# Kernel optimization log

Hardware: AMD Instinct MI355X
Metric: run time of the kernel (lower is better)

## Reference

```python
import jax, jax.numpy as jnp
import numpy as np

HEADS, DIM_HEAD, LANDMARKS, PINV_ITERS, RES_K = 8, 64, 256, 6, 33
DIM = 512


def layer_norm(x, w, b, eps=1e-5):
    mu = x.mean(-1, keepdims=True)
    var = ((x - mu) ** 2).mean(-1, keepdims=True)
    return (x - mu) * jax.lax.rsqrt(var + eps) * w + b


def moore_penrose_pinv(x, iters=PINV_ITERS):
    # x: (b, h, m, m)
    abs_x = jnp.abs(x)
    col = abs_x.sum(-1)
    row = abs_x.sum(-2)
    z = jnp.swapaxes(x, -1, -2) / (jnp.max(col) * jnp.max(row))
    I = jnp.eye(x.shape[-1], dtype=x.dtype)
    for _ in range(iters):
        xz = x @ z
        z = 0.25 * z @ (13.0 * I - xz @ (15.0 * I - xz @ (7.0 * I - xz)))
    return z


def nystrom_attention(x, qkv_w, out_w, out_b, res_kernel):
    b, n, _ = x.shape
    h, dh, m = HEADS, DIM_HEAD, LANDMARKS
    l = n // m  # seq chosen divisible by landmarks
    qkv = x @ qkv_w  # (b, n, 3*h*dh)
    q, k, v = jnp.split(qkv, 3, axis=-1)
    def to_heads(t):
        return t.reshape(b, n, h, dh).transpose(0, 2, 1, 3)  # (b,h,n,dh)
    q, k, v = to_heads(q), to_heads(k), to_heads(v)
    q = q * (dh ** -0.5)
    # landmark pooling: mean over contiguous groups of size l
    q_l = q.reshape(b, h, m, l, dh).mean(axis=3)  # (b,h,m,dh)
    k_l = k.reshape(b, h, m, l, dh).mean(axis=3)
    attn1 = jax.nn.softmax(jnp.einsum('bhid,bhjd->bhij', q, k_l), axis=-1)   # (b,h,n,m)
    attn2 = jax.nn.softmax(jnp.einsum('bhid,bhjd->bhij', q_l, k_l), axis=-1) # (b,h,m,m)
    attn3 = jax.nn.softmax(jnp.einsum('bhid,bhjd->bhij', q_l, k), axis=-1)   # (b,h,m,n)
    attn2_inv = moore_penrose_pinv(attn2)
    out = (attn1 @ attn2_inv) @ (attn3 @ v)  # (b,h,n,dh)
    # depthwise residual conv over sequence dim, per head
    pad = (RES_K - 1) // 2
    out = out + jax.lax.conv_general_dilated(
        v, res_kernel, window_strides=(1, 1), padding=((pad, pad), (0, 0)),
        dimension_numbers=('NCHW', 'OIHW', 'NCHW'), feature_group_count=h)
    out = out.transpose(0, 2, 1, 3).reshape(b, n, h * dh)
    return out @ out_w + out_b


def trans_layer(x, p):
    return x + nystrom_attention(layer_norm(x, p['norm_w'], p['norm_b']),
                                 p['qkv_w'], p['out_w'], p['out_b'], p['res_k'])


def setup_inputs() -> dict:
    key = jax.random.key(0)
    ks = jax.random.split(key, 20)
    N, F = 16383, 1024
    d = {}
    d['x'] = jax.random.normal(ks[0], (1, N, F), dtype=jnp.float32)
    d['fc_w'] = jax.random.normal(ks[1], (F, DIM), dtype=jnp.float32) * 0.03
    d['fc_b'] = jnp.zeros((DIM,), dtype=jnp.float32)
    d['cls_token'] = jax.random.normal(ks[2], (1, 1, DIM), dtype=jnp.float32) * 1e-6
    for i, base in [(3, 'l1'), (9, 'l2')]:
        d[base + '_norm_w'] = jnp.ones((DIM,), dtype=jnp.float32)
        d[base + '_norm_b'] = jnp.zeros((DIM,), dtype=jnp.float32)
        d[base + '_qkv_w'] = jax.random.normal(ks[i], (DIM, 3 * DIM), dtype=jnp.float32) * 0.03
        d[base + '_out_w'] = jax.random.normal(ks[i + 1], (DIM, DIM), dtype=jnp.float32) * 0.03
        d[base + '_out_b'] = jnp.zeros((DIM,), dtype=jnp.float32)
        d[base + '_res_k'] = jax.random.normal(ks[i + 2], (HEADS, 1, RES_K, 1), dtype=jnp.float32) * 0.1
    d['norm_w'] = jnp.ones((DIM,), dtype=jnp.float32)
    d['norm_b'] = jnp.zeros((DIM,), dtype=jnp.float32)
    d['clf_w'] = jax.random.normal(ks[15], (DIM, 4), dtype=jnp.float32) * 0.05
    d['clf_b'] = jnp.zeros((4,), dtype=jnp.float32)
    return d


def reference(x, fc_w, fc_b, cls_token, l1_norm_w, l1_norm_b, l1_qkv_w, l1_out_w,
              l1_out_b, l1_res_k, l2_norm_w, l2_norm_b, l2_qkv_w, l2_out_w,
              l2_out_b, l2_res_k, norm_w, norm_b, clf_w, clf_b):
    h = jax.nn.relu(x @ fc_w + fc_b)                       # (1, N, 512)
    h = jnp.concatenate([cls_token, h], axis=1)            # (1, N+1, 512)
    p1 = dict(norm_w=l1_norm_w, norm_b=l1_norm_b, qkv_w=l1_qkv_w,
              out_w=l1_out_w, out_b=l1_out_b, res_k=l1_res_k)
    p2 = dict(norm_w=l2_norm_w, norm_b=l2_norm_b, qkv_w=l2_qkv_w,
              out_w=l2_out_w, out_b=l2_out_b, res_k=l2_res_k)
    h = trans_layer(h, p1)
    h = trans_layer(h, p2)
    h = layer_norm(h, norm_w, norm_b)[:, 0]                # (1, 512)
    logits = h @ clf_w + clf_b                             # (1, n_classes)
    hazards = jax.nn.sigmoid(logits)
    S = jnp.cumprod(1.0 - hazards, axis=1)
    return (hazards, S)
```

## Files before the change

kernel.cpp:

```cpp
#include <hip/hip_runtime.h>

#define NTOK 16384
#define NDIM 512
#define STP_LD 280

typedef __attribute__((ext_vector_type(8))) short short8;
typedef __attribute__((ext_vector_type(4))) float f32x4;

__device__ __forceinline__ unsigned short f2bf(float f) {
  unsigned u = __float_as_uint(f);
  u += 0x7fffu + ((u >> 16) & 1u);
  return (unsigned short)(u >> 16);
}
__device__ __forceinline__ float bf2f(unsigned short u) {
  return __uint_as_float((unsigned)u << 16);
}

__device__ __forceinline__ void gload_lds16(const void* g, void* l) {
  __builtin_amdgcn_global_load_lds(
      (const __attribute__((address_space(1))) unsigned int*)(unsigned long long)(g),
      (__attribute__((address_space(3))) unsigned int*)(unsigned long long)(l), 16, 0, 0);
}

template<int EPI>
__global__ __launch_bounds__(256) void gemm_bf16(
    const unsigned short* __restrict__ A, const unsigned short* __restrict__ Bt,
    float* __restrict__ C, const float* __restrict__ bias,
    int M, int N, int K, int Mstore)
{
  __shared__ unsigned short As[2][128 * 32];
  __shared__ unsigned short Bs[2][128 * 32];
  const int tid = threadIdx.x;
  const int id = blockIdx.y * gridDim.x + blockIdx.x;
  const int nwg8 = (gridDim.x * gridDim.y) >> 3;
  const int logical = (id & 7) * nwg8 + (id >> 3);
  const int row0 = (logical / gridDim.x) * 128;
  const int col0 = (logical % gridDim.x) * 128;
  const int wave = tid >> 6, lane = tid & 63;
  const int wm = (wave >> 1) * 64, wn = (wave & 1) * 64;
  const int quad = lane >> 4, m16 = lane & 15;

  const int r0 = tid >> 2;
  const int c8 = (tid & 3) * 8;
  const unsigned short* Ag0 = A + (size_t)(row0 + r0) * K + c8;
  const unsigned short* Ag1 = A + (size_t)(row0 + r0 + 64) * K + c8;
  const unsigned short* Bg0 = Bt + (size_t)(col0 + r0) * K + c8;
  const unsigned short* Bg1 = Bt + (size_t)(col0 + r0 + 64) * K + c8;
  char* AsB = (char*)As;
  char* BsB = (char*)Bs;
  const int wb = wave * 1024;

  f32x4 acc[4][4] = {};
  const int nc = K >> 5;
  gload_lds16(Ag0, AsB + wb);
  gload_lds16(Ag1, AsB + 4096 + wb);
  gload_lds16(Bg0, BsB + wb);
  gload_lds16(Bg1, BsB + 4096 + wb);
  __syncthreads();
  int b = 0;
  for (int c = 0; c < nc; c++) {
    if (c + 1 < nc) {
      int k1 = (c + 1) * 32;
      gload_lds16(Ag0 + k1, AsB + (b ^ 1) * 8192 + wb);
      gload_lds16(Ag1 + k1, AsB + (b ^ 1) * 8192 + 4096 + wb);
      gload_lds16(Bg0 + k1, BsB + (b ^ 1) * 8192 + wb);
      gload_lds16(Bg1 + k1, BsB + (b ^ 1) * 8192 + 4096 + wb);
    }
    short8 af[4], bf[4];
#pragma unroll
    for (int i = 0; i < 4; i++) {
      af[i] = *(const short8*)&As[b][(wm + i * 16 + m16) * 32 + quad * 8];
      bf[i] = *(const short8*)&Bs[b][(wn + i * 16 + m16) * 32 + quad * 8];
    }
#pragma unroll
    for (int i = 0; i < 4; i++)
#pragma unroll
      for (int j = 0; j < 4; j++)
        acc[i][j] = __builtin_amdgcn_mfma_f32_16x16x32_bf16(af[i], bf[j], acc[i][j], 0, 0, 0);
    __syncthreads();
    b ^= 1;
  }
#pragma unroll
  for (int i = 0; i < 4; i++) {
#pragma unroll
    for (int r = 0; r < 4; r++) {
      int gr = row0 + wm + i * 16 + quad * 4 + r;
      if (gr < Mstore) {
#pragma unroll
        for (int j = 0; j < 4; j++) {
          int gc = col0 + wn + j * 16 + m16;
          float v = acc[i][j][r];
          if (EPI == 1) { v += bias[gc]; v = fmaxf(v, 0.f); }
          if (EPI == 2) { v += bias[gc] + C[(size_t)gr * N + gc]; }
          C[(size_t)gr * N + gc] = v;
        }
      }
    }
  }
}

__global__ __launch_bounds__(256) void qkv_gemm(
    const unsigned short* __restrict__ A, const unsigned short* __restrict__ Bt,
    unsigned short* __restrict__ qb, unsigned short* __restrict__ kb,
    unsigned short* __restrict__ vTb,
    float* __restrict__ q_l, float* __restrict__ k_lT,
    unsigned short* __restrict__ q_lb, unsigned short* __restrict__ k_lb)
{
  __shared__ unsigned short smem[17408];
  unsigned short* AsU = smem;
  unsigned short* BsU = smem + 8192;
  unsigned short* vt  = smem;
  const int tid = threadIdx.x;
  const int id = blockIdx.y * gridDim.x + blockIdx.x;
  const int nwg8 = (gridDim.x * gridDim.y) >> 3;
  const int logical = (id & 7) * nwg8 + (id >> 3);
  const int bx = logical % 12, by = logical / 12;
  const int row0 = by * 128, col0 = bx * 128;
  const int wave = tid >> 6, lane = tid & 63;
  const int wm = (wave >> 1) * 64, wn = (wave & 1) * 64;
  const int quad = lane >> 4, m16 = lane & 15;

  const int r0 = tid >> 2;
  const int c8 = (tid & 3) * 8;
  const unsigned short* Ag0 = A + (size_t)(row0 + r0) * 512 + c8;
  const unsigned short* Ag1 = A + (size_t)(row0 + r0 + 64) * 512 + c8;
  const unsigned short* Bg0 = Bt + (size_t)(col0 + r0) * 512 + c8;
  const unsigned short* Bg1 = Bt + (size_t)(col0 + r0 + 64) * 512 + c8;
  char* AsB = (char*)AsU;
  char* BsB = (char*)BsU;
  const int wb = wave * 1024;

  f32x4 acc[4][4] = {};
  gload_lds16(Ag0, AsB + wb);
  gload_lds16(Ag1, AsB + 4096 + wb);
  gload_lds16(Bg0, BsB + wb);
  gload_lds16(Bg1, BsB + 4096 + wb);
  __syncthreads();
  int b = 0;
  for (int c = 0; c < 16; c++) {
    if (c < 15) {
      int k1 = (c + 1) * 32;
      gload_lds16(Ag0 + k1, AsB + (b ^ 1) * 8192 + wb);
      gload_lds16(Ag1 + k1, AsB + (b ^ 1) * 8192 + 4096 + wb);
      gload_lds16(Bg0 + k1, BsB + (b ^ 1) * 8192 + wb);
      gload_lds16(Bg1 + k1, BsB + (b ^ 1) * 8192 + 4096 + wb);
    }
    short8 af[4], bf[4];
#pragma unroll
    for (int i = 0; i < 4; i++) {
      af[i] = *(const short8*)&AsU[b * 4096 + (wm + i * 16 + m16) * 32 + quad * 8];
      bf[i] = *(const short8*)&BsU[b * 4096 + (wn + i * 16 + m16) * 32 + quad * 8];
    }
#pragma unroll
    for (int i = 0; i < 4; i++)
#pragma unroll
      for (int j = 0; j < 4; j++)
        acc[i][j] = __builtin_amdgcn_mfma_f32_16x16x32_bf16(af[i], bf[j], acc[i][j], 0, 0, 0);
    __syncthreads();
    b ^= 1;
  }

  const int sel = bx >> 2;
  if (sel == 2) {
#pragma unroll
    for (int i = 0; i < 4; i++)
#pragma unroll
      for (int j = 0; j < 4; j++) {
        int c_l = wn + j * 16 + m16;
        int r_b = wm + i * 16 + quad * 4;
        ushort4 o;
        o.x = f2bf(acc[i][j][0]); o.y = f2bf(acc[i][j][1]);
        o.z = f2bf(acc[i][j][2]); o.w = f2bf(acc[i][j][3]);
        *(ushort4*)&vt[c_l * 136 + r_b] = o;
      }
    __syncthreads();
    const int gc0 = col0 - 1024;
    const int u = tid & 15, cc = tid >> 4;
#pragma unroll
    for (int pass = 0; pass < 8; pass++) {
      int c = pass * 16 + cc;
      short8 v8 = *(const short8*)&vt[c * 136 + u * 8];
      *(short8*)(vTb + (size_t)(gc0 + c) * NTOK + row0 + u * 8) = v8;
    }
  } else {
    const bool isq = (sel == 0);
    const float mul = isq ? 0.125f : 1.f;
#pragma unroll
    for (int i = 0; i < 4; i++)
#pragma unroll
      for (int j = 0; j < 4; j++) {
        int lc = wn + j * 16 + m16;
#pragma unroll
        for (int r = 0; r < 4; r++) {
          int lr = wm + i * 16 + quad * 4 + r;
          vt[lr * 136 + lc] = f2bf(acc[i][j][r] * mul);
        }
      }
    float ps[4];
#pragma unroll
    for (int j = 0; j < 4; j++) {
      float s = 0.f;
#pragma unroll
      for (int i = 0; i < 4; i++)
#pragma unroll
        for (int r = 0; r < 4; r++) s += acc[i][j][r];
      s += __shfl_xor(s, 16);
      s += __shfl_xor(s, 32);
      ps[j] = s;
    }
    if (quad == 0) {
      const int jg = by * 2 + (wm >> 6);
      const float sc = isq ? (0.125f / 64.f) : (1.f / 64.f);
#pragma unroll
      for (int j = 0; j < 4; j++) {
        int gc = col0 + wn + j * 16 + m16 - (isq ? 0 : 512);
        int hh = gc >> 6, d = gc & 63;
        float p = ps[j] * sc;
        if (isq) {
          size_t o = ((size_t)(hh * 256 + jg)) * 64 + d;
          q_l[o] = p;
          q_lb[o] = f2bf(p);
        } else {
          k_lT[((size_t)hh * 64 + d) * 256 + jg] = p;
          size_t of = ((size_t)hh << 14) + (jg >> 6) * 4096 + (d >> 5) * 2048
                    + ((jg >> 4) & 3) * 512 + ((d >> 3) & 3) * 128 + (jg & 15) * 8 + (d & 7);
          k_lb[of] = f2bf(p);
        }
      }
    }
    __syncthreads();
    unsigned short* ob = isq ? (qb + (size_t)row0 * 512 + col0)
                             : (kb + (size_t)row0 * 512 + (col0 - 512));
    const int u = tid & 15, cc = tid >> 4;
#pragma unroll
    for (int pass = 0; pass < 8; pass++) {
      int rloc = pass * 16 + cc;
      short8 v8 = *(const short8*)&vt[rloc * 136 + u * 8];
      *(short8*)(ob + (size_t)rloc * 512 + u * 8) = v8;
    }
  }
}

template<bool WN, bool WT, bool WF>
__global__ __launch_bounds__(256) void bmm_pinv64(
    const unsigned short* __restrict__ A, const unsigned short* __restrict__ Bt,
    unsigned short* __restrict__ Cn, unsigned short* __restrict__ Ct,
    float* __restrict__ Cf,
    float an, float bn, float at, float bt)
{
  const int hh = blockIdx.z;
  A  += (size_t)hh << 16;
  Bt += (size_t)hh << 16;
  __shared__ unsigned short As[2][64 * 32];
  __shared__ unsigned short Bs[2][64 * 32];
  const int tid = threadIdx.x;
  const int row0 = blockIdx.y * 64, col0 = blockIdx.x * 64;
  const int wave = tid >> 6, lane = tid & 63;
  const int wm = (wave >> 1) * 32, wn = (wave & 1) * 32;
  const int quad = lane >> 4, m16 = lane & 15;
  const int sr = wave * 16 + (lane >> 2);
  const int sc = (lane & 3) * 8;
  const unsigned short* Ag = A + (size_t)(row0 + sr) * 256 + sc;
  const unsigned short* Bg = Bt + (size_t)(col0 + sr) * 256 + sc;
  char* AsW = (char*)As + wave * 1024;
  char* BsW = (char*)Bs + wave * 1024;

  f32x4 acc[2][2] = {};
  gload_lds16(Ag, AsW);
  gload_lds16(Bg, BsW);
  __syncthreads();
  int b = 0;
  for (int c = 0; c < 8; c++) {
    if (c < 7) {
      gload_lds16(Ag + (c + 1) * 32, AsW + (b ^ 1) * 4096);
      gload_lds16(Bg + (c + 1) * 32, BsW + (b ^ 1) * 4096);
    }
    short8 af[2], bfr[2];
#pragma unroll
    for (int i = 0; i < 2; i++) {
      af[i]  = *(const short8*)&As[b][(wm + i * 16 + m16) * 32 + quad * 8];
      bfr[i] = *(const short8*)&Bs[b][(wn + i * 16 + m16) * 32 + quad * 8];
    }
#pragma unroll
    for (int i = 0; i < 2; i++)
#pragma unroll
      for (int j = 0; j < 2; j++)
        acc[i][j] = __builtin_amdgcn_mfma_f32_16x16x32_bf16(af[i], bfr[j], acc[i][j], 0, 0, 0);
    __syncthreads();
    b ^= 1;
  }
  unsigned short* CnH = Cn + ((size_t)hh << 16);
  unsigned short* CtH = Ct + ((size_t)hh << 16);
  float* CfH = WF ? (Cf + ((size_t)hh << 16)) : nullptr;
#pragma unroll
  for (int i = 0; i < 2; i++) {
#pragma unroll
    for (int r = 0; r < 4; r++) {
      int gr = row0 + wm + i * 16 + quad * 4 + r;
#pragma unroll
      for (int j = 0; j < 2; j++) {
        int gc = col0 + wn + j * 16 + m16;
        float p = acc[i][j][r];
        float diag = (gr == gc) ? 1.f : 0.f;
        if (WN) {
          unsigned short nb_ = f2bf(an * p + bn * diag);
          CnH[(size_t)gr * 256 + gc] = nb_;
          if (WF) CfH[(size_t)gr * 256 + gc] = bf2f(nb_);
        }
        if (WT) CtH[(size_t)gc * 256 + gr] = f2bf(at * p + bt * diag);
      }
    }
  }
}

__global__ void castpad_x(const float* __restrict__ x, unsigned short* __restrict__ xb,
                          size_t nvalid, const float* __restrict__ cls,
                          float* __restrict__ h) {
  size_t i4 = ((size_t)blockIdx.x * 256 + threadIdx.x) * 4;
  float4 v = make_float4(0.f, 0.f, 0.f, 0.f);
  if (i4 < nvalid) v = *(const float4*)(x + i4);
  ushort4 o;
  o.x = f2bf(v.x); o.y = f2bf(v.y); o.z = f2bf(v.z); o.w = f2bf(v.w);
  *(ushort4*)(xb + i4) = o;
  if (blockIdx.x == 0 && threadIdx.x < 128)
    *(float4*)(h + threadIdx.x * 4) = *(const float4*)(cls + threadIdx.x * 4);
}

__global__ __launch_bounds__(256) void transpose_cast(
    const float* __restrict__ in, unsigned short* __restrict__ out, int R, int C)
{
  __shared__ float tile[32][33];
  int r0 = blockIdx.x * 32, c0 = blockIdx.y * 32;
  int tx = threadIdx.x & 31, ty = threadIdx.x >> 5;
  for (int yy = ty; yy < 32; yy += 8)
    tile[yy][tx] = in[(size_t)(r0 + yy) * C + c0 + tx];
  __syncthreads();
  for (int yy = ty; yy < 32; yy += 8)
    out[(size_t)(c0 + yy) * R + r0 + tx] = f2bf(tile[tx][yy]);
}

__global__ __launch_bounds__(256) void conv_seq(
    const unsigned short* __restrict__ vTb, const float* __restrict__ res_k,
    unsigned short* __restrict__ convT)
{
  const int c = blockIdx.y;
  const int h = c >> 6;
  const int i0 = (blockIdx.x * 256 + threadIdx.x) * 8;
  float rk[33];
#pragma unroll
  for (int u = 0; u < 33; u++) rk[u] = res_k[h * 33 + u];
  const unsigned short* vr = vTb + (size_t)c * NTOK;
  float win[40];
#pragma unroll
  for (int ch = 0; ch < 5; ch++) {
    int a = i0 - 16 + ch * 8;
    if (a >= 0 && a < NTOK) {
      ushort4 u0 = *(const ushort4*)(vr + a);
      ushort4 u1 = *(const ushort4*)(vr + a + 4);
      win[ch * 8 + 0] = bf2f(u0.x); win[ch * 8 + 1] = bf2f(u0.y);
      win[ch * 8 + 2] = bf2f(u0.z); win[ch * 8 + 3] = bf2f(u0.w);
      win[ch * 8 + 4] = bf2f(u1.x); win[ch * 8 + 5] = bf2f(u1.y);
      win[ch * 8 + 6] = bf2f(u1.z); win[ch * 8 + 7] = bf2f(u1.w);
    } else {
#pragma unroll
      for (int u = 0; u < 8; u++) win[ch * 8 + u] = 0.f;
    }
  }
  ushort4 o0, o1;
  float out[8];
#pragma unroll
  for (int jj = 0; jj < 8; jj++) {
    float s = 0.f;
#pragma unroll
    for (int u = 0; u < 33; u++) s += rk[u] * win[jj + u];
    out[jj] = s;
  }
  o0.x = f2bf(out[0]); o0.y = f2bf(out[1]); o0.z = f2bf(out[2]); o0.w = f2bf(out[3]);
  o1.x = f2bf(out[4]); o1.y = f2bf(out[5]); o1.z = f2bf(out[6]); o1.w = f2bf(out[7]);
  *(ushort4*)(convT + (size_t)c * NTOK + i0) = o0;
  *(ushort4*)(convT + (size_t)c * NTOK + i0 + 4) = o1;
}

template<bool W2>
__global__ __launch_bounds__(256) void bmm_f32(
    const float* __restrict__ A, const float* __restrict__ B, float* __restrict__ C,
    float* __restrict__ C2, int M, int N, int K, float alpha, float beta, float gamma)
{
  const int h = blockIdx.z;
  A += (size_t)h * M * K; B += (size_t)h * K * N;
  size_t cb = (size_t)h * M * N;
  __shared__ float As[16][64];
  __shared__ float Bs[16][64];
  const int tid = threadIdx.x;
  const int row0 = blockIdx.y * 64, col0 = blockIdx.x * 64;
  const int ty = tid >> 4, tx = tid & 15;
  const int ar = tid >> 2, ac = (tid & 3) << 2;
  const int bk = tid >> 4, bj = (tid & 15) << 2;
  float acc[4][4] = {};
  float4 a  = *(const float4*)(A + (size_t)(row0 + ar) * K + ac);
  float4 bv = *(const float4*)(B + (size_t)bk * N + col0 + bj);
  for (int k0 = 0; k0 < K; k0 += 16) {
    As[ac + 0][ar] = a.x; As[ac + 1][ar] = a.y; As[ac + 2][ar] = a.z; As[ac + 3][ar] = a.w;
    *(float4*)&Bs[bk][bj] = bv;
    __syncthreads();
    if (k0 + 16 < K) {
      a  = *(const float4*)(A + (size_t)(row0 + ar) * K + k0 + 16 + ac);
      bv = *(const float4*)(B + (size_t)(k0 + 16 + bk) * N + col0 + bj);
    }
#pragma unroll
    for (int kk = 0; kk < 16; kk++) {
      float4 av = *(float4*)&As[kk][ty << 2];
      float4 bvv = *(float4*)&Bs[kk][tx << 2];
      float a4[4] = {av.x, av.y, av.z, av.w};
      float b4[4] = {bvv.x, bvv.y, bvv.z, bvv.w};
#pragma unroll
      for (int ii = 0; ii < 4; ii++)
#pragma unroll
        for (int jj = 0; jj < 4; jj++) acc[ii][jj] += a4[ii] * b4[jj];
    }
    __syncthreads();
  }
#pragma unroll
  for (int ii = 0; ii < 4; ii++) {
    int gr = row0 + (ty << 2) + ii;
#pragma unroll
    for (int jj = 0; jj < 4; jj++) {
      int gc = col0 + (tx << 2) + jj;
      float diag = (gr == gc) ? 1.f : 0.f;
      float v = alpha * acc[ii][jj] + beta * diag;
      C[cb + (size_t)gr * N + gc] = v;
      if (W2) C2[cb + (size_t)gr * N + gc] = gamma * diag - v;
    }
  }
}

__global__ __launch_bounds__(256) void layernorm_rows(
    const float* __restrict__ x, unsigned short* __restrict__ y,
    const float* __restrict__ w, const float* __restrict__ b)
{
  const int row = blockIdx.x, tid = threadIdx.x;
  const float* xr = x + (size_t)row * NDIM;
  float2 v = ((const float2*)xr)[tid];
  float sum = v.x + v.y, sq = v.x * v.x + v.y * v.y;
#pragma unroll
  for (int off = 32; off; off >>= 1) { sum += __shfl_xor(sum, off); sq += __shfl_xor(sq, off); }
  __shared__ float r1[4], r2[4];
  if ((tid & 63) == 0) { r1[tid >> 6] = sum; r2[tid >> 6] = sq; }
  __syncthreads();
  sum = r1[0] + r1[1] + r1[2] + r1[3];
  sq  = r2[0] + r2[1] + r2[2] + r2[3];
  float mu = sum * (1.f / 512.f);
  float var = sq * (1.f / 512.f) - mu * mu;
  float rs = rsqrtf(var + 1e-5f);
  float a = (v.x - mu) * rs * w[2 * tid]     + b[2 * tid];
  float c = (v.y - mu) * rs * w[2 * tid + 1] + b[2 * tid + 1];
  ((unsigned*)(y + (size_t)row * NDIM))[tid] = (unsigned)f2bf(a) | ((unsigned)f2bf(c) << 16);
}

__global__ __launch_bounds__(256) void attn2_softmax(
    const float* __restrict__ q_l, const float* __restrict__ k_lT,
    float* __restrict__ x2, unsigned short* __restrict__ x2b)
{
  int row = blockIdx.x, h = blockIdx.y, j = threadIdx.x;
// ... 124 lines not shown

  FF_STAGE(0, 0);
  __syncthreads();
  int b = 0;
  for (int c = 0; c < 8; c++) {
    if (c < 7) FF_STAGE(b ^ 1, c + 1);
    const unsigned short* Kb = Ks[b];
    const unsigned short* Vb = Vs[b];
    f32x4 s[4] = {};
    __builtin_amdgcn_s_setprio(1);
#pragma unroll
    for (int kt = 0; kt < 4; kt++) {
      const unsigned short* krow = Kb + ((kt << 4) + m16) * 64;
      short8 b0 = *(const short8*)(krow + co0);
      short8 b1 = *(const short8*)(krow + co1);
      s[kt] = __builtin_amdgcn_mfma_f32_16x16x32_bf16(aq0, b0, s[kt], 0, 0, 0);
      s[kt] = __builtin_amdgcn_mfma_f32_16x16x32_bf16(aq1, b1, s[kt], 0, 0, 0);
    }
    __builtin_amdgcn_s_setprio(0);
#pragma unroll
    for (int e = 0; e < 4; e++) {
      float mx = fmaxf(fmaxf(s[0][e], s[1][e]), fmaxf(s[2][e], s[3][e]));
      mx = fmaxf(mx, __shfl_xor(mx, 1));
      mx = fmaxf(mx, __shfl_xor(mx, 2));
      mx = fmaxf(mx, __shfl_xor(mx, 4));
      mx = fmaxf(mx, __shfl_xor(mx, 8));
      float mn = fmaxf(m_e[e], mx);
      float scale = __expf(m_e[e] - mn);
      m_e[e] = mn;
      float sum = 0.f;
#pragma unroll
      for (int kt = 0; kt < 4; kt++) {
        float ev = __expf(s[kt][e] - mn);
        s[kt][e] = ev;
        sum += ev;
      }
      sum += __shfl_xor(sum, 1); sum += __shfl_xor(sum, 2);
      sum += __shfl_xor(sum, 4); sum += __shfl_xor(sum, 8);
      l_e[e] = l_e[e] * scale + sum;
#pragma unroll
      for (int dt = 0; dt < 4; dt++) acc_o[dt][e] *= scale;
    }
#pragma unroll
    for (int kt = 0; kt < 4; kt++)
#pragma unroll
      for (int e = 0; e < 4; e++)
        pbuf[(quad * 4 + e) * 72 + kt * 16 + m16] = f2bf(s[kt][e]);
    asm volatile("s_waitcnt lgkmcnt(0)" ::: "memory");
    short8 ap0 = *(const short8*)&pbuf[m16 * 72 + quad * 8];
    short8 ap1 = *(const short8*)&pbuf[m16 * 72 + 32 + quad * 8];
    __builtin_amdgcn_s_setprio(1);
#pragma unroll
    for (int dt = 0; dt < 4; dt++) {
      const unsigned short* vrow = Vb + ((dt << 4) + m16) * 64;
      short8 bv0 = *(const short8*)(vrow + co0);
      short8 bv1 = *(const short8*)(vrow + co1);
      acc_o[dt] = __builtin_amdgcn_mfma_f32_16x16x32_bf16(ap0, bv0, acc_o[dt], 0, 0, 0);
      acc_o[dt] = __builtin_amdgcn_mfma_f32_16x16x32_bf16(ap1, bv1, acc_o[dt], 0, 0, 0);
    }
    __builtin_amdgcn_s_setprio(0);
    __syncthreads();
    b ^= 1;
  }
#undef FF_STAGE
  float* ob = Opart + ((size_t)(ks * 8 + h) * 256 + qrow_w) * 64;
#pragma unroll
  for (int dt = 0; dt < 4; dt++)
#pragma unroll
    for (int e = 0; e < 4; e++)
      ob[(size_t)(quad * 4 + e) * 64 + dt * 16 + m16] = acc_o[dt][e];
  if (m16 == 0) {
    float* mlb = mlpart + ((size_t)(ks * 8 + h) * 256 + qrow_w) * 2;
#pragma unroll
    for (int e = 0; e < 4; e++) {
      mlb[(quad * 4 + e) * 2]     = m_e[e];
      mlb[(quad * 4 + e) * 2 + 1] = l_e[e];
    }
  }
}

__global__ __launch_bounds__(256) void flash_merge(
    const float* __restrict__ Opart, const float* __restrict__ mlpart,
    float* __restrict__ kv)
{
  const int rc = blockIdx.x, h = blockIdx.y, tid = threadIdx.x;
  const int r = rc * 32 + (tid >> 3);
  const int d0 = (tid & 7) * 8;
  float M = -1e30f;
  for (int ks = 0; ks < 32; ks++)
    M = fmaxf(M, mlpart[((size_t)(ks * 8 + h) * 256 + r) * 2]);
  float L = 0.f;
  float o[8];
#pragma unroll
  for (int j = 0; j < 8; j++) o[j] = 0.f;
  for (int ks = 0; ks < 32; ks++) {
    const float* mlb = mlpart + ((size_t)(ks * 8 + h) * 256 + r) * 2;
    float w = __expf(mlb[0] - M);
    L += mlb[1] * w;
    const float* op = Opart + ((size_t)(ks * 8 + h) * 256 + r) * 64 + d0;
    float4 a = *(const float4*)op;
    float4 b = *(const float4*)(op + 4);
    o[0] += a.x * w; o[1] += a.y * w; o[2] += a.z * w; o[3] += a.w * w;
    o[4] += b.x * w; o[5] += b.y * w; o[6] += b.z * w; o[7] += b.w * w;
  }
  float invL = 1.f / L;
  float* out = kv + ((size_t)(h * 256 + r)) * 64 + d0;
#pragma unroll
  for (int j = 0; j < 8; j++) out[j] = o[j] * invL;
}

__global__ __launch_bounds__(256) void bmt_kernel(
    const float* __restrict__ zf, const float* __restrict__ kv,
    unsigned short* __restrict__ BmT)
{
  const int jb = blockIdx.x, hh = blockIdx.y, tid = threadIdx.x;
  __shared__ float zt[64 * 256];
  const float* zsrc = zf + ((size_t)hh << 16) + (size_t)(jb * 64) * 256;
  for (int rep = 0; rep < 16; rep++) {
    int e4 = (rep * 256 + tid) * 4;
    *(float4*)&zt[e4] = *(const float4*)(zsrc + e4);
  }
  __syncthreads();
  const int d = tid & 63, jg = tid >> 6;
  const float* kvh = kv + ((size_t)hh << 14) + d;
  float acc[16];
#pragma unroll
  for (int u = 0; u < 16; u++) acc[u] = 0.f;
  for (int k0 = 0; k0 < 256; k0 += 8) {
    float kv8[8];
#pragma unroll
    for (int u = 0; u < 8; u++) kv8[u] = kvh[(size_t)(k0 + u) << 6];
#pragma unroll
    for (int jj = 0; jj < 16; jj++) {
      const float* zr = &zt[(jg * 16 + jj) * 256 + k0];
#pragma unroll
      for (int u = 0; u < 8; u++) acc[jj] += zr[u] * kv8[u];
    }
  }
  unsigned short* obh = BmT + ((size_t)hh << 14) + (d >> 5) * 8192
                        + ((d >> 4) & 1) * 512 + (d & 15) * 8;
#pragma unroll
  for (int jj = 0; jj < 16; jj++) {
    int j = jb * 64 + jg * 16 + jj;
    obh[(j >> 5) * 1024 + ((j >> 3) & 3) * 128 + (j & 7)] = f2bf(acc[jj]);
  }
}

__global__ __launch_bounds__(256) void attn1_out(
    const unsigned short* __restrict__ qb, const unsigned short* __restrict__ k_lb,
    const unsigned short* __restrict__ BmT, const unsigned short* __restrict__ convT,
    unsigned short* __restrict__ attn_out)
{
  const int qc = blockIdx.x, h = blockIdx.y, tid = threadIdx.x;
  const int q0 = qc * 32;
  const int wave = tid >> 6, lane = tid & 63;
  const int quad = lane >> 4, m16 = lane & 15;

  __shared__ unsigned short stp[32 * STP_LD];
  __shared__ float redm[4][32], redl[4][32];

  const int mi3 = (wave & 1) * 16;
  const int nbase = (wave >> 1) * 32;
  const int gi0 = q0 + mi3 + quad * 4;
  ushort4 cv4_[2];
#pragma unroll
  for (int t = 0; t < 2; t++) {
    int d = nbase + t * 16 + m16;
    cv4_[t] = *(const ushort4*)(convT + (size_t)((h << 6) + d) * NTOK + gi0);
  }

  f32x4 acc1[2][4] = {};
  {
    const unsigned short* qbase = qb + (size_t)q0 * 512 + (h << 6);
    const unsigned short* kf = k_lb + ((size_t)h << 14) + (wave << 12);
#pragma unroll
    for (int kc = 0; kc < 2; kc++) {
      short8 aq[2], bk[4];
#pragma unroll
      for (int i = 0; i < 2; i++)
        aq[i] = *(const short8*)(qbase + (size_t)(i * 16 + m16) * 512 + kc * 32 + quad * 8);
#pragma unroll
      for (int n = 0; n < 4; n++)
        bk[n] = *(const short8*)(kf + kc * 2048 + n * 512 + lane * 8);
#pragma unroll
      for (int i = 0; i < 2; i++)
#pragma unroll
        for (int n = 0; n < 4; n++)
          acc1[i][n] = __builtin_amdgcn_mfma_f32_16x16x32_bf16(aq[i], bk[n], acc1[i][n], 0, 0, 0);
    }
  }
#pragma unroll
  for (int i = 0; i < 2; i++) {
#pragma unroll
    for (int e = 0; e < 4; e++) {
      float mx = fmaxf(fmaxf(acc1[i][0][e], acc1[i][1][e]), fmaxf(acc1[i][2][e], acc1[i][3][e]));
      mx = fmaxf(mx, __shfl_xor(mx, 1));
      mx = fmaxf(mx, __shfl_xor(mx, 2));
      mx = fmaxf(mx, __shfl_xor(mx, 4));
      mx = fmaxf(mx, __shfl_xor(mx, 8));
      if (m16 == 0) redm[wave][i * 16 + quad * 4 + e] = mx;
    }
  }
  __syncthreads();
#pragma unroll
  for (int i = 0; i < 2; i++) {
#pragma unroll
    for (int e = 0; e < 4; e++) {
      int r = i * 16 + quad * 4 + e;
      float gm = fmaxf(fmaxf(redm[0][r], redm[1][r]), fmaxf(redm[2][r], redm[3][r]));
      float s = 0.f;
#pragma unroll
      for (int n = 0; n < 4; n++) {
        float ev = __expf(acc1[i][n][e] - gm);
        acc1[i][n][e] = ev;
        s += ev;
      }
      s += __shfl_xor(s, 1); s += __shfl_xor(s, 2);
      s += __shfl_xor(s, 4); s += __shfl_xor(s, 8);
      if (m16 == 0) redl[wave][r] = s;
    }
  }
#pragma unroll
  for (int i = 0; i < 2; i++)
#pragma unroll
    for (int n = 0; n < 4; n++) {
      int col = wave * 64 + n * 16 + m16;
#pragma unroll
      for (int e = 0; e < 4; e++)
        stp[(i * 16 + quad * 4 + e) * STP_LD + col] = f2bf(acc1[i][n][e]);
    }
  __syncthreads();

  f32x4 acc3[2] = {};
  {
    const unsigned short* bf_ = BmT + ((size_t)h << 14) + ((nbase >> 5) << 13);
#pragma unroll
    for (int kc = 0; kc < 8; kc++) {
      short8 ap = *(const short8*)&stp[(mi3 + m16) * STP_LD + kc * 32 + quad * 8];
#pragma unroll
      for (int t = 0; t < 2; t++) {
        short8 bp = *(const short8*)(bf_ + kc * 1024 + t * 512 + lane * 8);
        acc3[t] = __builtin_amdgcn_mfma_f32_16x16x32_bf16(ap, bp, acc3[t], 0, 0, 0);
      }
    }
  }
#pragma unroll
  for (int t = 0; t < 2; t++) {
    int d = nbase + t * 16 + m16;
    unsigned short cvs[4] = {cv4_[t].x, cv4_[t].y, cv4_[t].z, cv4_[t].w};
#pragma unroll
    for (int e = 0; e < 4; e++) {
      int lr = mi3 + quad * 4 + e;
      float l = redl[0][lr] + redl[1][lr] + redl[2][lr] + redl[3][lr];
      float v = acc3[t][e] / l + bf2f(cvs[e]);
      attn_out[((size_t)(gi0 + e) << 9) + (h << 6) + d] = f2bf(v);
    }
  }
}

__global__ __launch_bounds__(256) void final_head(
    const float* __restrict__ hrow, const float* __restrict__ nw, const float* __restrict__ nb,
    const float* __restrict__ cw, const float* __restrict__ cb, float* __restrict__ out)
{
  const int tid = threadIdx.x;
  __shared__ float ln0[512];
  __shared__ float r1[4], r2[4];
  __shared__ float lg[4][4];
  float2 v = ((const float2*)hrow)[tid];
  float sum = v.x + v.y, sq = v.x * v.x + v.y * v.y;
#pragma unroll
  for (int off = 32; off; off >>= 1) { sum += __shfl_xor(sum, off); sq += __shfl_xor(sq, off); }
  if ((tid & 63) == 0) { r1[tid >> 6] = sum; r2[tid >> 6] = sq; }
  __syncthreads();
  sum = r1[0] + r1[1] + r1[2] + r1[3];
  sq  = r2[0] + r2[1] + r2[2] + r2[3];
  float mu = sum * (1.f / 512.f);
  float var = sq * (1.f / 512.f) - mu * mu;
  float rs = rsqrtf(var + 1e-5f);
  ln0[2 * tid]     = (v.x - mu) * rs * nw[2 * tid]     + nb[2 * tid];
  ln0[2 * tid + 1] = (v.y - mu) * rs * nw[2 * tid + 1] + nb[2 * tid + 1];
  __syncthreads();
  float p[4] = {0.f, 0.f, 0.f, 0.f};
  for (int k = tid; k < 512; k += 256) {
    float lv = ln0[k];
#pragma unroll
    for (int c = 0; c < 4; c++) p[c] += lv * cw[k * 4 + c];
  }
#pragma unroll
  for (int off = 32; off; off >>= 1)
#pragma unroll
    for (int c = 0; c < 4; c++) p[c] += __shfl_xor(p[c], off);
  if ((tid & 63) == 0) {
    int w = tid >> 6;
#pragma unroll
    for (int c = 0; c < 4; c++) lg[w][c] = p[c];
  }
  __syncthreads();
  if (tid == 0) {
    float cum = 1.f;
    for (int c = 0; c < 4; c++) {
      float logit = lg[0][c] + lg[1][c] + lg[2][c] + lg[3][c] + cb[c];
      float hz = 1.f / (1.f + __expf(-logit));
      out[c] = hz;
      cum *= (1.f - hz);
      out[4 + c] = cum;
    }
  }
}

extern "C" void kernel_launch(void* const* d_in, const int* in_sizes, int n_in,
                              void* d_out, int out_size, void* d_ws, size_t ws_size,
                              hipStream_t stream)
{
  (void)in_sizes; (void)n_in; (void)out_size; (void)ws_size;
  const float* x    = (const float*)d_in[0];
  const float* fc_w = (const float*)d_in[1];
  const float* fc_b = (const float*)d_in[2];
  const float* cls  = (const float*)d_in[3];
  const float* nw[2]   = {(const float*)d_in[4],  (const float*)d_in[10]};
  const float* nb[2]   = {(const float*)d_in[5],  (const float*)d_in[11]};
  const float* qkvw[2] = {(const float*)d_in[6],  (const float*)d_in[12]};
  const float* outw[2] = {(const float*)d_in[7],  (const float*)d_in[13]};
  const float* outb[2] = {(const float*)d_in[8],  (const float*)d_in[14]};
  const float* resk[2] = {(const float*)d_in[9],  (const float*)d_in[15]};
  const float* fnw = (const float*)d_in[16];
  const float* fnb = (const float*)d_in[17];
  const float* cw  = (const float*)d_in[18];
  const float* cb  = (const float*)d_in[19];

  float* ws = (float*)d_ws;
  float* h    = ws; ws += (size_t)NTOK * NDIM;
  float* qkv  = ws; ws += (size_t)NTOK * 1536;
  float* bigv = ws; ws += (size_t)(512 * NTOK) / 2;
  float* q_l  = ws; ws += 8 * 256 * 64;
  float* k_lT = ws; ws += 8 * 256 * 64;
  float* x2   = ws; ws += 8 * 256 * 256;
  float* zf   = ws; ws += 8 * 256 * 256;
  float* zfin = ws; ws += 8 * 256 * 256;
  float* tA   = ws; ws += 8 * 256 * 256;
  float* tB   = ws; ws += 8 * 256 * 256;
  float* tC   = ws; ws += 8 * 256 * 256;
  float* kv   = ws; ws += 8 * 256 * 64;
  float* scal = ws; ws += 64;
  unsigned short* actb = (unsigned short*)ws; ws += (size_t)NTOK * NDIM / 2;
  unsigned short* wT   = (unsigned short*)ws; ws += (1536 * 512) / 2;
  unsigned short* qb   = (unsigned short*)ws; ws += (size_t)NTOK * NDIM / 2;
  unsigned short* k_lb = (unsigned short*)ws; ws += (8 * 256 * 64) / 2;
  unsigned short* q_lb = (unsigned short*)ws; ws += (8 * 256 * 64) / 2;
  unsigned short* x2b  = (unsigned short*)ws; ws += (8 * 256 * 256) / 2;
  unsigned short* zb0  = (unsigned short*)ws; ws += (8 * 256 * 256) / 2;
  unsigned short* zb1  = (unsigned short*)ws; ws += (8 * 256 * 256) / 2;
  unsigned short* zT0  = (unsigned short*)ws; ws += (8 * 256 * 256) / 2;
  unsigned short* zT1  = (unsigned short*)ws; ws += (8 * 256 * 256) / 2;
  unsigned short* xzb  = (unsigned short*)ws; ws += (8 * 256 * 256) / 2;
  unsigned short* t1T  = (unsigned short*)ws; ws += (8 * 256 * 256) / 2;
  unsigned short* t2T  = (unsigned short*)ws; ws += (8 * 256 * 256) / 2;
  unsigned short* t3T  = (unsigned short*)ws; ws += (8 * 256 * 256) / 2;
  unsigned short* BmT  = (unsigned short*)ws; ws += (8 * 64 * 256) / 2;
  unsigned short* kbuf = (unsigned short*)ws; ws += (size_t)NTOK * NDIM / 2;

  unsigned short* xb  = (unsigned short*)qkv;
  unsigned short* vTb = (unsigned short*)bigv;
  float* Opart  = qkv;
  float* mlpart = qkv + (size_t)32 * 8 * 256 * 64;
  unsigned short* convT = (unsigned short*)(qkv + (size_t)32 * 8 * 256 * 64 + 32 * 8 * 256 * 2);

  unsigned short* zbp[2] = {zb0, zb1};
  unsigned short* zTp[2] = {zT0, zT1};

  castpad_x<<<16384, 256, 0, stream>>>(x, xb, (size_t)16383 * 1024, cls, h);
  transpose_cast<<<dim3(32, 16), 256, 0, stream>>>(fc_w, wT, 1024, 512);
  gemm_bf16<1><<<dim3(4, 128), 256, 0, stream>>>(xb, wT, h + 512, fc_b,
                                                 16384, 512, 1024, 16383);

  for (int L = 0; L < 2; L++) {
    layernorm_rows<<<NTOK, 256, 0, stream>>>(h, actb, nw[L], nb[L]);
    transpose_cast<<<dim3(16, 48), 256, 0, stream>>>(qkvw[L], wT, 512, 1536);
    qkv_gemm<<<dim3(12, 128), 256, 0, stream>>>(actb, wT, qb, kbuf, vTb,
                                                q_l, k_lT, q_lb, k_lb);
    attn2_softmax<<<dim3(256, 8), 256, 0, stream>>>(q_l, k_lT, x2, x2b);
    colrow_max<<<dim3(8, 2), 256, 0, stream>>>(x2, scal);
    zinit_bf<<<2048, 256, 0, stream>>>(x2, zbp[0], zTp[0], scal);

    flash_fused<<<dim3(32, 4, 8), 256, 0, stream>>>(q_lb, kbuf, vTb, Opart, mlpart);
    flash_merge<<<dim3(8, 8), 256, 0, stream>>>(Opart, mlpart, kv);
    conv_seq<<<dim3(8, 512), 256, 0, stream>>>(vTb, resk[L], convT);

    int cur = 0;
    dim3 pg(4, 4, 8);
    for (int it = 0; it < 5; it++) {
      bmm_pinv64<true,  true, false><<<pg, 256, 0, stream>>>(x2b, zTp[cur], xzb, t1T, nullptr,
                                                             1.f, 0.f, -1.f, 7.f);
      bmm_pinv64<false, true, false><<<pg, 256, 0, stream>>>(xzb, t1T, nullptr, t2T, nullptr,
                                                             0.f, 0.f, -1.f, 15.f);
      bmm_pinv64<false, true, false><<<pg, 256, 0, stream>>>(xzb, t2T, nullptr, t3T, nullptr,
                                                             0.f, 0.f, -1.f, 13.f);
      if (it < 4)
        bmm_pinv64<true, true, false><<<pg, 256, 0, stream>>>(zbp[cur], t3T, zbp[cur ^ 1],
                                                              zTp[cur ^ 1], nullptr,
                                                              0.25f, 0.f, 0.25f, 0.f);
      else
        bmm_pinv64<true, true, true><<<pg, 256, 0, stream>>>(zbp[cur], t3T, zbp[cur ^ 1],
                                                             zTp[cur ^ 1], zf,
                                                             0.25f, 0.f, 0.25f, 0.f);
      cur ^= 1;
    }
    bmm_f32<true ><<<dim3(4, 4, 8), 256, 0, stream>>>(x2, zf, tA, tB, 256, 256, 256, 1.f, 0.f, 7.f);
    bmm_f32<false><<<dim3(4, 4, 8), 256, 0, stream>>>(tA, tB, tC, nullptr, 256, 256, 256, -1.f, 15.f, 0.f);
    bmm_f32<false><<<dim3(4, 4, 8), 256, 0, stream>>>(tA, tC, tB, nullptr, 256, 256, 256, -1.f, 13.f, 0.f);
    bmm_f32<false><<<dim3(4, 4, 8), 256, 0, stream>>>(zf, tB, zfin, nullptr, 256, 256, 256, 0.25f, 0.f, 0.f);

    bmt_kernel<<<dim3(4, 8), 256, 0, stream>>>(zfin, kv, BmT);
    attn1_out<<<dim3(512, 8), 256, 0, stream>>>(qb, k_lb, BmT, convT, actb);
    transpose_cast<<<dim3(16, 16), 256, 0, stream>>>(outw[L], wT, 512, 512);
    gemm_bf16<2><<<dim3(4, 128), 256, 0, stream>>>(actb, wT, h, outb[L],
                                                   16384, 512, 512, NTOK);
  }
  final_head<<<1, 256, 0, stream>>>(h, fnw, fnb, cw, cb, (float*)d_out);
}
```

Baseline: 930.8 us.

## Rework pinv bmm to full-K swizzled LDS tiles and per-wave attn1 rows

The pinv batched matmul now loads the full K=256 panel of A (64 rows) and B (32 cols) into LDS at once, using an XOR swizzle to avoid bank conflicts. It drops the double-buffered K loop and its per-step barriers, and launches twice as many blocks so more of the GPU is busy. attn1_out is restructured so each wave owns 16 query rows across all 256 landmarks. This lets the softmax reductions stay within the wave, removing cross-wave LDS reductions and block barriers. The trade-offs are more LDS per block, higher register pressure from 16 score tiles, and repeated loading of k_l and BmT by each wave.

Result: no change. 915.0 us (-1.7%).

```diff
diff --git a/kernel.cpp b/kernel.cpp
--- a/kernel.cpp
+++ b/kernel.cpp
@@ -2,7 +2,6 @@
 
 #define NTOK 16384
 #define NDIM 512
-#define STP_LD 280
 
 typedef __attribute__((ext_vector_type(8))) short short8;
 typedef __attribute__((ext_vector_type(4))) float f32x4;
@@ -251,64 +250,56 @@
   const int hh = blockIdx.z;
   A  += (size_t)hh << 16;
   Bt += (size_t)hh << 16;
-  __shared__ unsigned short As[2][64 * 32];
-  __shared__ unsigned short Bs[2][64 * 32];
+  __shared__ unsigned short As[64 * 256];
+  __shared__ unsigned short Bs[32 * 256];
   const int tid = threadIdx.x;
-  const int row0 = blockIdx.y * 64, col0 = blockIdx.x * 64;
+  const int row0 = blockIdx.y * 64, col0 = blockIdx.x * 32;
   const int wave = tid >> 6, lane = tid & 63;
-  const int wm = (wave >> 1) * 32, wn = (wave & 1) * 32;
+  const int wm = (wave >> 1) * 32, wn = (wave & 1) * 16;
   const int quad = lane >> 4, m16 = lane & 15;
-  const int sr = wave * 16 + (lane >> 2);
-  const int sc = (lane & 3) * 8;
-  const unsigned short* Ag = A + (size_t)(row0 + sr) * 256 + sc;
-  const unsigned short* Bg = Bt + (size_t)(col0 + sr) * 256 + sc;
-  char* AsW = (char*)As + wave * 1024;
-  char* BsW = (char*)Bs + wave * 1024;
-
-  f32x4 acc[2][2] = {};
-  gload_lds16(Ag, AsW);
-  gload_lds16(Bg, BsW);
-  __syncthreads();
-  int b = 0;
-  for (int c = 0; c < 8; c++) {
-    if (c < 7) {
-      gload_lds16(Ag + (c + 1) * 32, AsW + (b ^ 1) * 4096);
-      gload_lds16(Bg + (c + 1) * 32, BsW + (b ^ 1) * 4096);
-    }
-    short8 af[2], bfr[2];
-#pragma unroll
-    for (int i = 0; i < 2; i++) {
-      af[i]  = *(const short8*)&As[b][(wm + i * 16 + m16) * 32 + quad * 8];
-      bfr[i] = *(const short8*)&Bs[b][(wn + i * 16 + m16) * 32 + quad * 8];
-    }
-#pragma unroll
-    for (int i = 0; i < 2; i++)
-#pragma unroll
-      for (int j = 0; j < 2; j++)
-        acc[i][j] = __builtin_amdgcn_mfma_f32_16x16x32_bf16(af[i], bfr[j], acc[i][j], 0, 0, 0);
-    __syncthreads();
-    b ^= 1;
+
+  const int rl  = wave * 2 + (lane >> 5);
+  const int cs_ = ((lane & 31) ^ rl) * 8;
+  const unsigned short* Ag = A + (size_t)(row0 + rl) * 256 + cs_;
+  const unsigned short* Bg = Bt + (size_t)(col0 + rl) * 256 + cs_;
+  char* AsB = (char*)As;
+  char* BsB = (char*)Bs;
+#pragma unroll
+  for (int p = 0; p < 8; p++)
+    gload_lds16(Ag + (size_t)p * 8 * 256, AsB + p * 4096 + wave * 1024);
+#pragma unroll
+  for (int q = 0; q < 4; q++)
+    gload_lds16(Bg + (size_t)q * 8 * 256, BsB + q * 4096 + wave * 1024);
+  __syncthreads();
+
+  const int xs = m16 & 7;
+  f32x4 acc[2] = {};
+#pragma unroll
+  for (int kc = 0; kc < 8; kc++) {
+    int g = (kc * 4 + quad) ^ xs;
+    short8 af0 = *(const short8*)&As[(wm + m16) * 256 + g * 8];
+    short8 af1 = *(const short8*)&As[(wm + 16 + m16) * 256 + g * 8];
+    short8 bfr = *(const short8*)&Bs[(wn + m16) * 256 + g * 8];
+    acc[0] = __builtin_amdgcn_mfma_f32_16x16x32_bf16(af0, bfr, acc[0], 0, 0, 0);
+    acc[1] = __builtin_amdgcn_mfma_f32_16x16x32_bf16(af1, bfr, acc[1], 0, 0, 0);
   }
   unsigned short* CnH = Cn + ((size_t)hh << 16);
   unsigned short* CtH = Ct + ((size_t)hh << 16);
   float* CfH = WF ? (Cf + ((size_t)hh << 16)) : nullptr;
+  const int gc = col0 + wn + m16;
 #pragma unroll
   for (int i = 0; i < 2; i++) {
 #pragma unroll
     for (int r = 0; r < 4; r++) {
       int gr = row0 + wm + i * 16 + quad * 4 + r;
-#pragma unroll
-      for (int j = 0; j < 2; j++) {
-        int gc = col0 + wn + j * 16 + m16;
-        float p = acc[i][j][r];
-        float diag = (gr == gc) ? 1.f : 0.f;
-        if (WN) {
-          unsigned short nb_ = f2bf(an * p + bn * diag);
-          CnH[(size_t)gr * 256 + gc] = nb_;
-          if (WF) CfH[(size_t)gr * 256 + gc] = bf2f(nb_);
-        }
-        if (WT) CtH[(size_t)gc * 256 + gr] = f2bf(at * p + bt * diag);
+      float p = acc[i][r];
+      float diag = (gr == gc) ? 1.f : 0.f;
+      if (WN) {
+        unsigned short nb_ = f2bf(an * p + bn * diag);
+        CnH[(size_t)gr * 256 + gc] = nb_;
+        if (WF) CfH[(size_t)gr * 256 + gc] = bf2f(nb_);
       }
+      if (WT) CtH[(size_t)gc * 256 + gr] = f2bf(at * p + bt * diag);
     }
   }
 }
@@ -739,107 +730,86 @@
     unsigned short* __restrict__ attn_out)
 {
   const int qc = blockIdx.x, h = blockIdx.y, tid = threadIdx.x;
-  const int q0 = qc * 32;
   const int wave = tid >> 6, lane = tid & 63;
   const int quad = lane >> 4, m16 = lane & 15;
-
-  __shared__ unsigned short stp[32 * STP_LD];
-  __shared__ float redm[4][32], redl[4][32];
-
-  const int mi3 = (wave & 1) * 16;
-  const int nbase = (wave >> 1) * 32;
-  const int gi0 = q0 + mi3 + quad * 4;
-  ushort4 cv4_[2];
-#pragma unroll
-  for (int t = 0; t < 2; t++) {
-    int d = nbase + t * 16 + m16;
-    cv4_[t] = *(const ushort4*)(convT + (size_t)((h << 6) + d) * NTOK + gi0);
-  }
-
-  f32x4 acc1[2][4] = {};
-  {
-    const unsigned short* qbase = qb + (size_t)q0 * 512 + (h << 6);
-    const unsigned short* kf = k_lb + ((size_t)h << 14) + (wave << 12);
-#pragma unroll
-    for (int kc = 0; kc < 2; kc++) {
-      short8 aq[2], bk[4];
-#pragma unroll
-      for (int i = 0; i < 2; i++)
-        aq[i] = *(const short8*)(qbase + (size_t)(i * 16 + m16) * 512 + kc * 32 + quad * 8);
-#pragma unroll
-      for (int n = 0; n < 4; n++)
-        bk[n] = *(const short8*)(kf + kc * 2048 + n * 512 + lane * 8);
-#pragma unroll
-      for (int i = 0; i < 2; i++)
-#pragma unroll
-        for (int n = 0; n < 4; n++)
-          acc1[i][n] = __builtin_amdgcn_mfma_f32_16x16x32_bf16(aq[i], bk[n], acc1[i][n], 0, 0, 0);
-    }
-  }
-#pragma unroll
-  for (int i = 0; i < 2; i++) {
+  const int q0 = qc * 64 + wave * 16;
+
+  __shared__ unsigned short pbuf_all[4][16 * 264];
+  unsigned short* pbuf = pbuf_all[wave];
+
+  const int gi0 = q0 + quad * 4;
+  ushort4 cv4_[4];
+#pragma unroll
+  for (int dt = 0; dt < 4; dt++) {
+    int d = dt * 16 + m16;
+    cv4_[dt] = *(const ushort4*)(convT + (size_t)((h << 6) + d) * NTOK + gi0);
+  }
+
+  const unsigned short* qbase = qb + (size_t)(q0 + m16) * 512 + (h << 6);
+  short8 aq0 = *(const short8*)(qbase + quad * 8);
+  short8 aq1 = *(const short8*)(qbase + 32 + quad * 8);
+
+  const unsigned short* kh = k_lb + ((size_t)h << 14);
+  f32x4 s[16];
+#pragma unroll
+  for (int jt = 0; jt < 16; jt++) {
+    const unsigned short* kf = kh + (jt >> 2) * 4096 + (jt & 3) * 512 + lane * 8;
+    short8 b0 = *(const short8*)(kf);
+    short8 b1 = *(const short8*)(kf + 2048);
+    f32x4 z = {};
+    z = __builtin_amdgcn_mfma_f32_16x16x32_bf16(aq0, b0, z, 0, 0, 0);
+    z = __builtin_amdgcn_mfma_f32_16x16x32_bf16(aq1, b1, z, 0, 0, 0);
+    s[jt] = z;
+  }
+
+  float l_e[4];
+#pragma unroll
+  for (int e = 0; e < 4; e++) {
+    float mx = s[0][e];
+#pragma unroll
+    for (int jt = 1; jt < 16; jt++) mx = fmaxf(mx, s[jt][e]);
+    mx = fmaxf(mx, __shfl_xor(mx, 1));
+    mx = fmaxf(mx, __shfl_xor(mx, 2));
+    mx = fmaxf(mx, __shfl_xor(mx, 4));
+    mx = fmaxf(mx, __shfl_xor(mx, 8));
+    float sum = 0.f;
+#pragma unroll
+    for (int jt = 0; jt < 16; jt++) {
+      float ev = __expf(s[jt][e] - mx);
+      s[jt][e] = ev;
+      sum += ev;
+    }
+    sum += __shfl_xor(sum, 1); sum += __shfl_xor(sum, 2);
+    sum += __shfl_xor(sum, 4); sum += __shfl_xor(sum, 8);
+    l_e[e] = sum;
+  }
+
+#pragma unroll
+  for (int jt = 0; jt < 16; jt++)
+#pragma unroll
+    for (int e = 0; e < 4; e++)
+      pbuf[(quad * 4 + e) * 264 + jt * 16 + m16] = f2bf(s[jt][e]);
+  asm volatile("s_waitcnt lgkmcnt(0)" ::: "memory");
+
+  const unsigned short* bmh = BmT + ((size_t)h << 14);
+  f32x4 acc_o[4] = {};
+#pragma unroll
+  for (int kc = 0; kc < 8; kc++) {
+    short8 ap = *(const short8*)&pbuf[m16 * 264 + kc * 32 + quad * 8];
+#pragma unroll
+    for (int dt = 0; dt < 4; dt++) {
+      short8 bp = *(const short8*)(bmh + (dt >> 1) * 8192 + kc * 1024 + (dt & 1) * 512 + lane * 8);
+      acc_o[dt] = __builtin_amdgcn_mfma_f32_16x16x32_bf16(ap, bp, acc_o[dt], 0, 0, 0);
+    }
+  }
+
+#pragma unroll
+  for (int dt = 0; dt < 4; dt++) {
+    int d = dt * 16 + m16;
+    unsigned short cvs[4] = {cv4_[dt].x, cv4_[dt].y, cv4_[dt].z, cv4_[dt].w};
 #pragma unroll
     for (int e = 0; e < 4; e++) {
-      float mx = fmaxf(fmaxf(acc1[i][0][e], acc1[i][1][e]), fmaxf(acc1[i][2][e], acc1[i][3][e]));
-      mx = fmaxf(mx, __shfl_xor(mx, 1));
-      mx = fmaxf(mx, __shfl_xor(mx, 2));
-      mx = fmaxf(mx, __shfl_xor(mx, 4));
-      mx = fmaxf(mx, __shfl_xor(mx, 8));
-      if (m16 == 0) redm[wave][i * 16 + quad * 4 + e] = mx;
-    }
-  }
-  __syncthreads();
-#pragma unroll
-  for (int i = 0; i < 2; i++) {
-#pragma unroll
-    for (int e = 0; e < 4; e++) {
-      int r = i * 16 + quad * 4 + e;
-      float gm = fmaxf(fmaxf(redm[0][r], redm[1][r]), fmaxf(redm[2][r], redm[3][r]));
-      float s = 0.f;
-#pragma unroll
-      for (int n = 0; n < 4; n++) {
-        float ev = __expf(acc1[i][n][e] - gm);
-        acc1[i][n][e] = ev;
-        s += ev;
-      }
-      s += __shfl_xor(s, 1); s += __shfl_xor(s, 2);
-      s += __shfl_xor(s, 4); s += __shfl_xor(s, 8);
-      if (m16 == 0) redl[wave][r] = s;
-    }
-  }
-#pragma unroll
-  for (int i = 0; i < 2; i++)
-#pragma unroll
-    for (int n = 0; n < 4; n++) {
-      int col = wave * 64 + n * 16 + m16;
-#pragma unroll
-      for (int e = 0; e < 4; e++)
-        stp[(i * 16 + quad * 4 + e) * STP_LD + col] = f2bf(acc1[i][n][e]);
-    }
-  __syncthreads();
-
-  f32x4 acc3[2] = {};
-  {
-    const unsigned short* bf_ = BmT + ((size_t)h << 14) + ((nbase >> 5) << 13);
-#pragma unroll
-    for (int kc = 0; kc < 8; kc++) {
-      short8 ap = *(const short8*)&stp[(mi3 + m16) * STP_LD + kc * 32 + quad * 8];
-#pragma unroll
-      for (int t = 0; t < 2; t++) {
-        short8 bp = *(const short8*)(bf_ + kc * 1024 + t * 512 + lane * 8);
-        acc3[t] = __builtin_amdgcn_mfma_f32_16x16x32_bf16(ap, bp, acc3[t], 0, 0, 0);
-      }
-    }
-  }
-#pragma unroll
-  for (int t = 0; t < 2; t++) {
-    int d = nbase + t * 16 + m16;
-    unsigned short cvs[4] = {cv4_[t].x, cv4_[t].y, cv4_[t].z, cv4_[t].w};
-#pragma unroll
-    for (int e = 0; e < 4; e++) {
-      int lr = mi3 + quad * 4 + e;
-      float l = redl[0][lr] + redl[1][lr] + redl[2][lr] + redl[3][lr];
-      float v = acc3[t][e] / l + bf2f(cvs[e]);
+      float v = acc_o[dt][e] / l_e[e] + bf2f(cvs[e]);
       attn_out[((size_t)(gi0 + e) << 9) + (h << 6) + d] = f2bf(v);
     }
   }
@@ -974,7 +944,7 @@
     conv_seq<<<dim3(8, 512), 256, 0, stream>>>(vTb, resk[L], convT);
 
     int cur = 0;
-    dim3 pg(4, 4, 8);
+    dim3 pg(8, 4, 8);
     for (int it = 0; it < 5; it++) {
       bmm_pinv64<true,  true, false><<<pg, 256, 0, stream>>>(x2b, zTp[cur], xzb, t1T, nullptr,
                                                              1.f, 0.f, -1.f, 7.f);
@@ -998,7 +968,7 @@
     bmm_f32<false><<<dim3(4, 4, 8), 256, 0, stream>>>(zf, tB, zfin, nullptr, 256, 256, 256, 0.25f, 0.f, 0.f);
 
     bmt_kernel<<<dim3(4, 8), 256, 0, stream>>>(zfin, kv, BmT);
-    attn1_out<<<dim3(512, 8), 256, 0, stream>>>(qb, k_lb, BmT, convT, actb);
+    attn1_out<<<dim3(256, 8), 256, 0, stream>>>(qb, k_lb, BmT, convT, actb);
     transpose_cast<<<dim3(16, 16), 256, 0, stream>>>(outw[L], wT, 512, 512);
     gemm_bf16<2><<<dim3(4, 128), 256, 0, stream>>>(actb, wT, h, outb[L],
                                                    16384, 512, 512, NTOK);
```

## Load full-K tiles into swizzled LDS and halve pinv bmm output tile width

Applied to the files above, without the earlier changes.

The pinv batched matmul now stages the entire K=256 strip of A (64 rows) and Bt (32 rows) into LDS in one shot, using an XOR swizzle to avoid bank conflicts. This replaces the double-buffered 8-step K loop and its per-step barriers. The output tile shrinks from 64x64 to 64x32, doubling the grid to 256 blocks per launch so more CUs are busy on these small latency-bound matmuls. In exchange it uses more LDS per block (48KB) and re-reads A twice as often.

Result: faster. 880.4 us (-5.4%).

```diff
diff --git a/kernel.cpp b/kernel.cpp
--- a/kernel.cpp
+++ b/kernel.cpp
@@ -251,64 +251,56 @@
   const int hh = blockIdx.z;
   A  += (size_t)hh << 16;
   Bt += (size_t)hh << 16;
-  __shared__ unsigned short As[2][64 * 32];
-  __shared__ unsigned short Bs[2][64 * 32];
+  __shared__ unsigned short As[64 * 256];
+  __shared__ unsigned short Bs[32 * 256];
   const int tid = threadIdx.x;
-  const int row0 = blockIdx.y * 64, col0 = blockIdx.x * 64;
+  const int row0 = blockIdx.y * 64, col0 = blockIdx.x * 32;
   const int wave = tid >> 6, lane = tid & 63;
-  const int wm = (wave >> 1) * 32, wn = (wave & 1) * 32;
+  const int wm = (wave >> 1) * 32, wn = (wave & 1) * 16;
   const int quad = lane >> 4, m16 = lane & 15;
-  const int sr = wave * 16 + (lane >> 2);
-  const int sc = (lane & 3) * 8;
-  const unsigned short* Ag = A + (size_t)(row0 + sr) * 256 + sc;
-  const unsigned short* Bg = Bt + (size_t)(col0 + sr) * 256 + sc;
-  char* AsW = (char*)As + wave * 1024;
-  char* BsW = (char*)Bs + wave * 1024;
-
-  f32x4 acc[2][2] = {};
-  gload_lds16(Ag, AsW);
-  gload_lds16(Bg, BsW);
-  __syncthreads();
-  int b = 0;
-  for (int c = 0; c < 8; c++) {
-    if (c < 7) {
-      gload_lds16(Ag + (c + 1) * 32, AsW + (b ^ 1) * 4096);
-      gload_lds16(Bg + (c + 1) * 32, BsW + (b ^ 1) * 4096);
-    }
-    short8 af[2], bfr[2];
-#pragma unroll
-    for (int i = 0; i < 2; i++) {
-      af[i]  = *(const short8*)&As[b][(wm + i * 16 + m16) * 32 + quad * 8];
-      bfr[i] = *(const short8*)&Bs[b][(wn + i * 16 + m16) * 32 + quad * 8];
-    }
-#pragma unroll
-    for (int i = 0; i < 2; i++)
-#pragma unroll
-      for (int j = 0; j < 2; j++)
-        acc[i][j] = __builtin_amdgcn_mfma_f32_16x16x32_bf16(af[i], bfr[j], acc[i][j], 0, 0, 0);
-    __syncthreads();
-    b ^= 1;
+
+  const int rl  = wave * 2 + (lane >> 5);
+  const int cs_ = ((lane & 31) ^ rl) * 8;
+  const unsigned short* Ag = A + (size_t)(row0 + rl) * 256 + cs_;
+  const unsigned short* Bg = Bt + (size_t)(col0 + rl) * 256 + cs_;
+  char* AsB = (char*)As;
+  char* BsB = (char*)Bs;
+#pragma unroll
+  for (int p = 0; p < 8; p++)
+    gload_lds16(Ag + (size_t)p * 8 * 256, AsB + p * 4096 + wave * 1024);
+#pragma unroll
+  for (int q = 0; q < 4; q++)
+    gload_lds16(Bg + (size_t)q * 8 * 256, BsB + q * 4096 + wave * 1024);
+  __syncthreads();
+
+  const int xs = m16 & 7;
+  f32x4 acc[2] = {};
+#pragma unroll
+  for (int kc = 0; kc < 8; kc++) {
+    int g = (kc * 4 + quad) ^ xs;
+    short8 af0 = *(const short8*)&As[(wm + m16) * 256 + g * 8];
+    short8 af1 = *(const short8*)&As[(wm + 16 + m16) * 256 + g * 8];
+    short8 bfr = *(const short8*)&Bs[(wn + m16) * 256 + g * 8];
+    acc[0] = __builtin_amdgcn_mfma_f32_16x16x32_bf16(af0, bfr, acc[0], 0, 0, 0);
+    acc[1] = __builtin_amdgcn_mfma_f32_16x16x32_bf16(af1, bfr, acc[1], 0, 0, 0);
   }
   unsigned short* CnH = Cn + ((size_t)hh << 16);
   unsigned short* CtH = Ct + ((size_t)hh << 16);
   float* CfH = WF ? (Cf + ((size_t)hh << 16)) : nullptr;
+  const int gc = col0 + wn + m16;
 #pragma unroll
   for (int i = 0; i < 2; i++) {
 #pragma unroll
     for (int r = 0; r < 4; r++) {
       int gr = row0 + wm + i * 16 + quad * 4 + r;
-#pragma unroll
-      for (int j = 0; j < 2; j++) {
-        int gc = col0 + wn + j * 16 + m16;
-        float p = acc[i][j][r];
-        float diag = (gr == gc) ? 1.f : 0.f;
-        if (WN) {
-          unsigned short nb_ = f2bf(an * p + bn * diag);
-          CnH[(size_t)gr * 256 + gc] = nb_;
-          if (WF) CfH[(size_t)gr * 256 + gc] = bf2f(nb_);
-        }
-        if (WT) CtH[(size_t)gc * 256 + gr] = f2bf(at * p + bt * diag);
+      float p = acc[i][r];
+      float diag = (gr == gc) ? 1.f : 0.f;
+      if (WN) {
+        unsigned short nb_ = f2bf(an * p + bn * diag);
+        CnH[(size_t)gr * 256 + gc] = nb_;
+        if (WF) CfH[(size_t)gr * 256 + gc] = bf2f(nb_);
       }
+      if (WT) CtH[(size_t)gc * 256 + gr] = f2bf(at * p + bt * diag);
     }
   }
 }
@@ -974,7 +966,7 @@
     conv_seq<<<dim3(8, 512), 256, 0, stream>>>(vTb, resk[L], convT);
 
     int cur = 0;
-    dim3 pg(4, 4, 8);
+    dim3 pg(8, 4, 8);
     for (int it = 0; it < 5; it++) {
       bmm_pinv64<true,  true, false><<<pg, 256, 0, stream>>>(x2b, zTp[cur], xzb, t1T, nullptr,
                                                              1.f, 0.f, -1.f, 7.f);
```
